# Kernel tuning notes

Hardware: AMD Instinct MI355X
Metric: run time of the kernel (lower is better)

## Reference

```python
import jax, jax.numpy as jnp
import numpy as np

EMBED = 1024
HEADS = 16
HEAD_DIM = EMBED // HEADS


def setup_inputs() -> dict:
    key = jax.random.key(0)
    kx, kq, kk, kv, ko = jax.random.split(key, 5)
    s = 1.0 / np.sqrt(EMBED)
    return {
        "x": jax.random.normal(kx, (4, 2048, EMBED), dtype=jnp.float32),
        "Wq": jax.random.uniform(kq, (EMBED, EMBED), jnp.float32, -s, s),
        "Wk": jax.random.uniform(kk, (EMBED, EMBED), jnp.float32, -s, s),
        "Wv": jax.random.uniform(kv, (EMBED, EMBED), jnp.float32, -s, s),
        "Wo": jax.random.uniform(ko, (EMBED, EMBED), jnp.float32, -s, s),
    }


def reference(x, Wq, Wk, Wv, Wo):
    B, S, E = x.shape
    # nn.Linear computes x @ W.T; weights stored as (out, in)
    q = (x @ Wq.T).reshape(B, S, HEADS, HEAD_DIM).transpose(0, 2, 1, 3)  # [B,H,S,D]
    k = (x @ Wk.T).reshape(B, S, HEADS, HEAD_DIM).transpose(0, 2, 1, 3)
    v = (x @ Wv.T).reshape(B, S, HEADS, HEAD_DIM).transpose(0, 2, 1, 3)
    scores = jnp.einsum("bhsd,bhtd->bhst", q, k) / np.sqrt(HEAD_DIM)  # [B,H,S,S]
    causal = jnp.triu(jnp.ones((S, S), dtype=bool), k=1)
    scores = jnp.where(causal[None, None], -jnp.inf, scores)
    probs = jax.nn.softmax(scores, axis=-1)  # dropout_rate=0 -> identity
    attn = jnp.einsum("bhst,bhtd->bhsd", probs, v)  # [B,H,S,D]
    attn = attn.transpose(0, 2, 1, 3).reshape(B, S, E)
    return attn @ Wo.T
```

## Files before the change

kernel.cpp:

```cpp
#include <hip/hip_runtime.h>

#define EMB 1024
#define NHEADS 16
#define HD 64
#define BATCH 4
#define SEQ 2048
#define MTOK (BATCH*SEQ)

typedef __bf16 bf16x8 __attribute__((ext_vector_type(8)));
typedef __bf16 bf16x4 __attribute__((ext_vector_type(4)));
typedef float  f32x4  __attribute__((ext_vector_type(4)));

#define MFMA16(a,b,c) __builtin_amdgcn_mfma_f32_16x16x32_bf16(a,b,c,0,0,0)

__device__ __forceinline__ void gload_lds16(const __bf16* g, __bf16* l) {
    __builtin_amdgcn_global_load_lds(
        (__attribute__((address_space(1))) void*)(g),
        (__attribute__((address_space(3))) void*)(l), 16, 0, 0);
}

__global__ void cvt_all(const float* __restrict__ x,  const float* __restrict__ wq,
                        const float* __restrict__ wk, const float* __restrict__ wv,
                        const float* __restrict__ wo,
                        __bf16* xb, __bf16* wqb, __bf16* wkb, __bf16* wvb, __bf16* wob) {
    int z = blockIdx.y;
    const float* src = (z == 0) ? x : (z == 1) ? wq : (z == 2) ? wk : (z == 3) ? wv : wo;
    __bf16*      dst = (z == 0) ? xb : (z == 1) ? wqb : (z == 2) ? wkb : (z == 3) ? wvb : wob;
    int n = (z == 0) ? MTOK * EMB : EMB * EMB;
    int i = (blockIdx.x * blockDim.x + threadIdx.x) * 4;
    if (i < n) {
        float4 v = *(const float4*)(src + i);
        bf16x4 o = { (__bf16)v.x, (__bf16)v.y, (__bf16)v.z, (__bf16)v.w };
        *(bf16x4*)(dst + i) = o;
    }
}

__global__ __launch_bounds__(256) void transpose_v(const __bf16* __restrict__ vb,
                                                   __bf16* __restrict__ vt) {
    __shared__ __bf16 t[64 * 72];
    const int tid = threadIdx.x;
    const int bh = blockIdx.y, s0 = blockIdx.x * 64;
    const __bf16* src = vb + ((size_t)bh * SEQ + s0) * HD;
    int sr = tid >> 3, cc = (tid & 7) * 8;
    bf16x8 a0 = *(const bf16x8*)(src + (size_t)sr * HD + cc);
    bf16x8 a1 = *(const bf16x8*)(src + (size_t)(sr + 32) * HD + cc);
    *(bf16x8*)(t + sr * 72 + cc)        = a0;
    *(bf16x8*)(t + (sr + 32) * 72 + cc) = a1;
    __syncthreads();
    int dr = tid >> 3, g = tid & 7;
    __bf16* dstb = vt + (size_t)bh * HD * SEQ + s0;
    #pragma unroll
    for (int it = 0; it < 2; ++it) {
        int d = dr + it * 32;
        bf16x8 o;
        #pragma unroll
        for (int j = 0; j < 8; ++j) o[j] = t[(g * 8 + j) * 72 + d];
        *(bf16x8*)(dstb + (size_t)d * SEQ + g * 8) = o;
    }
}


#define SCHEDB() __builtin_amdgcn_sched_barrier(0)
#define PH_MID()                                                        \
    do { SCHEDB(); __builtin_amdgcn_s_barrier();                        \
         asm volatile("s_waitcnt lgkmcnt(0)" ::: "memory");             \
         SCHEDB(); __builtin_amdgcn_s_setprio(1); } while (0)
#define PH_END()                                                        \
    do { __builtin_amdgcn_s_setprio(0); SCHEDB();                       \
         __builtin_amdgcn_s_barrier(); SCHEDB(); } while (0)
#define PH_END_VM0()                                                    \
    do { __builtin_amdgcn_s_setprio(0); SCHEDB();                       \
         asm volatile("s_waitcnt vmcnt(0)" ::: "memory");               \
         __builtin_amdgcn_s_barrier(); SCHEDB(); } while (0)
#define PH_END_VM2()                                                    \
    do { __builtin_amdgcn_s_setprio(0); SCHEDB();                       \
         asm volatile("s_waitcnt vmcnt(2)" ::: "memory");               \
         __builtin_amdgcn_s_barrier(); SCHEDB(); } while (0)

#define MMAQ(AF, BF, MH, NHI)                                           \
    do {                                                                \
        _Pragma("unroll")                                               \
        for (int m_ = 0; m_ < 4; ++m_) {                                \
            _Pragma("unroll")                                           \
            for (int n_ = 0; n_ < NH; ++n_) {                           \
                f32x4 c_ = acc[(MH)*4 + m_][(NHI)*NH + n_];             \
                c_ = MFMA16(AF[m_][0], BF[n_][0], c_);                  \
                c_ = MFMA16(AF[m_][1], BF[n_][1], c_);                  \
                acc[(MH)*4 + m_][(NHI)*NH + n_] = c_;                   \
            }                                                           \
        }                                                               \
    } while (0)

template<int BN>
__device__ __forceinline__ void gemm8ph(
    const __bf16* __restrict__ Ag,
    const __bf16* __restrict__ Bg,
    __bf16* __restrict__ As, __bf16* __restrict__ Bs,
    f32x4 (&acc)[8][BN/64])
{
    constexpr int NH    = BN / 128;
    constexpr int BSLOT = BN * 64;

    const int tid   = threadIdx.x;
    const int w     = tid >> 6;
    const int mlane = tid & 15;
    const int quad  = (tid >> 4) & 3;
    const int wm    = w >> 2;
    const int wn    = w & 3;

    const int rho = mlane & 7;
    const int e0  = (quad ^ rho) * 8;
    const int aA0 = mlane * 64 + e0;
    const int aB0 = (wn * (BN / 4) + mlane) * 64 + e0;

    const int so = (tid >> 3) * 1024 + (((tid & 7) ^ ((tid >> 3) & 7)) * 8);
    const int sd = (tid & ~63) * 8;

    const auto stA = [&](int slot, int half, int kt) {
        const __bf16* g = Ag + half * 131072 + kt + so;
        __bf16* l = As + slot * 16384 + half * 8192 + sd;
        gload_lds16(g, l);
        gload_lds16(g + 65536, l + 4096);
    };
    const auto stB = [&](int slot, int half, int kt) {
        const __bf16* g = Bg + half * 131072 + kt + so;
        __bf16* l = Bs + slot * BSLOT + half * 8192 + sd;
        gload_lds16(g, l);
        gload_lds16(g + 65536, l + 4096);
    };
    const auto rdA = [&](bf16x8 (&dst)[4][2], int slot, int grp) {
        const __bf16* base = As + slot * 16384 + wm * 8192 + grp * 4096;
        #pragma unroll
        for (int m = 0; m < 4; ++m) {
            dst[m][0] = *(const bf16x8*)(base + m * 1024 + aA0);
            dst[m][1] = *(const bf16x8*)(base + m * 1024 + (aA0 ^ 32));
        }
    };
    const auto rdB = [&](bf16x8 (&dst)[NH][2], int slot, int nh) {
        const __bf16* base = Bs + slot * BSLOT + nh * (NH * 1024);
        #pragma unroll
        for (int n = 0; n < NH; ++n) {
            dst[n][0] = *(const bf16x8*)(base + n * 1024 + aB0);
            dst[n][1] = *(const bf16x8*)(base + n * 1024 + (aB0 ^ 32));
        }
    };

    const f32x4 fz = {0.f, 0.f, 0.f, 0.f};
    #pragma unroll
    for (int i = 0; i < 8; ++i)
        #pragma unroll
        for (int j = 0; j < BN / 64; ++j) acc[i][j] = fz;

    bf16x8 afA[4][2], afB[4][2], bfA[NH][2], bfB[NH][2];

    stA(0, 0, 0); stA(0, 1, 0); stB(0, 0, 0);
    if (BN == 256) stB(0, 1, 0);
    stA(1, 0, 64);
    asm volatile("s_waitcnt vmcnt(2)" ::: "memory");
    SCHEDB(); __builtin_amdgcn_s_barrier(); SCHEDB();

    #pragma unroll 1
    for (int t = 0; t < 8; ++t) {
        const bool last = (t == 7);
        const int ktc1 = t * 128 + 64;
        const int ktn0 = t * 128 + 128;
        const int ktn1 = t * 128 + 192;

        rdA(afA, 0, 0); rdB(bfA, 0, 0);
        stA(1, 1, ktc1);
        PH_MID(); MMAQ(afA, bfA, 0, 0); PH_END();

        rdB(bfB, 0, 1);
        stB(1, 0, ktc1);
        PH_MID(); MMAQ(afA, bfB, 0, 1); PH_END();

        rdA(afB, 0, 1);
        if (BN == 256) stB(1, 1, ktc1);
        PH_MID(); MMAQ(afB, bfB, 1, 1); PH_END();

        if (!last) stA(0, 0, ktn0);
        PH_MID(); MMAQ(afB, bfA, 1, 0);
        if (last) PH_END_VM0(); else PH_END_VM2();

        rdA(afA, 1, 0); rdB(bfA, 1, 0);
        if (!last) stA(0, 1, ktn0);
        PH_MID(); MMAQ(afA, bfA, 0, 0); PH_END();

        rdB(bfB, 1, 1);
        if (!last) stB(0, 0, ktn0);
        PH_MID(); MMAQ(afA, bfB, 0, 1); PH_END();

        rdA(afB, 1, 1);
        if (!last && BN == 256) stB(0, 1, ktn0);
        PH_MID(); MMAQ(afB, bfB, 1, 1); PH_END();

        if (!last) stA(1, 0, ktn1);
        PH_MID(); MMAQ(afB, bfA, 1, 0);
        if (last) PH_END(); else PH_END_VM2();
    }
}

__global__ __launch_bounds__(512, 2) void qkv_gemm(
    const __bf16* __restrict__ xb, const __bf16* __restrict__ wqkv,
    __bf16* __restrict__ Qb, __bf16* __restrict__ Kb, __bf16* __restrict__ Vb)
{
    __shared__ __bf16 As[2 * 256 * 64];
    __shared__ __bf16 Bs[2 * 256 * 64];

    const int bid   = blockIdx.x;
    const int local = bid >> 3;
    const int mt    = (bid & 7) * 4 + (local & 3);
    const int nt    = local >> 2;

    f32x4 acc[8][4];
    gemm8ph<256>(xb + (size_t)mt * 262144, wqkv + (size_t)nt * 262144, As, Bs, acc);

    const int tid = threadIdx.x, w = tid >> 6;
    const int mlane = tid & 15, quad = (tid >> 4) & 3;
    const int wm = w >> 2, wn = w & 3;
    const int rowb = mt * 256 + wm * 128;
    const int colb = nt * 256 + wn * 64;

    #pragma unroll
    for (int ni = 0; ni < 4; ++ni) {
        int gcol = colb + (ni >> 1) * 32 + (ni & 1) * 16 + mlane;
        int z = gcol >> 10, cc = gcol & 1023;
        int h = cc >> 6, d = cc & 63;
        __bf16* O = (z == 0) ? Qb : (z == 1) ? Kb : Vb;
        float scl = (z == 0) ? 0.18033688011112042f : 1.0f;
        #pragma unroll
        for (int mi = 0; mi < 8; ++mi) {
            int grow = rowb + (mi >> 2) * 64 + (mi & 3) * 16 + quad * 4;
            int b = grow >> 11, s = grow & 2047;
            #pragma unroll
            for (int r = 0; r < 4; ++r)
                O[(((size_t)b * NHEADS + h) * SEQ + (s + r)) * HD + d] =
                    (__bf16)(acc[mi][ni][r] * scl);
        }
    }
}

__global__ __launch_bounds__(512, 2) void out_gemm(
    const __bf16* __restrict__ attnb, const __bf16* __restrict__ wo,
    float* __restrict__ out)
{
    __shared__ __bf16 As[2 * 256 * 64];
    __shared__ __bf16 Bs[2 * 128 * 64];

    const int bid   = blockIdx.x;
    const int local = bid >> 3;
    const int mt    = (bid & 7) * 4 + (local & 3);
    const int nt    = local >> 2;

    f32x4 acc[8][2];
    gemm8ph<128>(attnb + (size_t)mt * 262144, wo + (size_t)nt * 131072, As, Bs, acc);

    const int tid = threadIdx.x, w = tid >> 6;
    const int mlane = tid & 15, quad = (tid >> 4) & 3;
    const int wm = w >> 2, wn = w & 3;
    const int rowb = mt * 256 + wm * 128;
    const int colb = nt * 128 + wn * 32;

    #pragma unroll
    for (int mi = 0; mi < 8; ++mi) {
        int grow = rowb + (mi >> 2) * 64 + (mi & 3) * 16 + quad * 4;
        #pragma unroll
        for (int ni = 0; ni < 2; ++ni) {
            int gcol = colb + ni * 16 + mlane;
            #pragma unroll
            for (int r = 0; r < 4; ++r)
                out[(size_t)(grow + r) * EMB + gcol] = acc[mi][ni][r];
        }
    }
}

__global__ __launch_bounds__(512, 1) void attn_kernel(
    const __bf16* __restrict__ Qb, const __bf16* __restrict__ Kb,
    const __bf16* __restrict__ Vtg, __bf16* __restrict__ attnb)
{
    __shared__ __bf16 Ks[2 * 64 * 64];
    __shared__ __bf16 Vs[2 * 64 * 64];
    __shared__ __bf16 Ps[8 * 16 * 72];

    const int tid = threadIdx.x, w = tid >> 6, lane = tid & 63;
    const int mlane = lane & 15, quad = lane >> 4;
    const int h = blockIdx.y, b = blockIdx.z;
    const size_t headoff = ((size_t)b * NHEADS + h) * SEQ * HD;
    const __bf16* Qg = Qb + headoff;
    const __bf16* Kg = Kb + headoff;
    const __bf16* Vg = Vtg + headoff;
    __bf16* Psw = Ps + w * 16 * 72;
    const int g0 = quad ^ (mlane & 7);
    const f32x4 fzero = {0.f, 0.f, 0.f, 0.f};

    const int st_row = tid >> 3;
    const int st_cc  = (tid & 7) ^ (st_row & 7);
    const int st_dst = (tid & ~63) * 8;

    for (int sp = 0; sp < 2; ++sp) {
        const int strip = sp ? (15 - (int)blockIdx.x) : (int)blockIdx.x;
        const int qw  = strip * 128 + w * 16;
        const int nch = 2 * strip + 2;

        __syncthreads();

        gload_lds16(Kg + (size_t)st_row * HD + st_cc * 8, Ks + st_dst);
        gload_lds16(Vg + (size_t)st_row * SEQ + st_cc * 8, Vs + st_dst);

        bf16x8 bq0 = *(const bf16x8*)(Qg + (size_t)(qw + mlane) * HD + quad * 8);
        bf16x8 bq1 = *(const bf16x8*)(Qg + (size_t)(qw + mlane) * HD + 32 + quad * 8);

        float l_acc = 0.f;
        f32x4 o[4];
        #pragma unroll
        for (int dt = 0; dt < 4; ++dt) o[dt] = fzero;

        for (int c = 0; c < nch; ++c) {
            const int tb = c * 64;
            const __bf16* Kp = Ks + (c & 1) * 4096;
            const __bf16* Vp = Vs + (c & 1) * 4096;
            __bf16* Kn = Ks + ((c & 1) ^ 1) * 4096;
            __bf16* Vn = Vs + ((c & 1) ^ 1) * 4096;

            asm volatile("s_waitcnt vmcnt(0)" ::: "memory");
            __syncthreads();

            if (c + 1 < nch) {
                const int tbn = tb + 64;
                gload_lds16(Kg + (size_t)(tbn + st_row) * HD + st_cc * 8, Kn + st_dst);
                gload_lds16(Vg + (size_t)st_row * SEQ + tbn + st_cc * 8, Vn + st_dst);
            }

            const int rel = qw + 15 - tb;
            if (rel >= 0) {
                f32x4 s[4];
                #pragma unroll
                for (int mt = 0; mt < 4; ++mt) {
                    const __bf16* ka = Kp + (mt * 16 + mlane) * 64;
                    bf16x8 ak0 = *(const bf16x8*)(ka + g0 * 8);
                    bf16x8 ak1 = *(const bf16x8*)(ka + (g0 ^ 4) * 8);
                    s[mt] = MFMA16(ak1, bq1, MFMA16(ak0, bq0, fzero));
                }
                if (rel < 78) {
                    const int qrel = qw + mlane - tb - quad * 4;
                    #pragma unroll
                    for (int mt = 0; mt < 4; ++mt)
                        #pragma unroll
                        for (int r = 0; r < 4; ++r)
                            if (mt * 16 + r > qrel) s[mt][r] = -3e38f;
                }

                f32x4 vsum = fzero;
                #pragma unroll
                for (int mt = 0; mt < 4; ++mt) {
                    #pragma unroll
                    for (int r = 0; r < 4; ++r)
                        s[mt][r] = __builtin_amdgcn_exp2f(s[mt][r]);
                    vsum += s[mt];
                    bf16x4 pb = { (__bf16)s[mt][0], (__bf16)s[mt][1],
                                  (__bf16)s[mt][2], (__bf16)s[mt][3] };
                    *(bf16x4*)(Psw + mlane * 72 + mt * 16 + quad * 4) = pb;
                }
                l_acc += (vsum[0] + vsum[1]) + (vsum[2] + vsum[3]);

                #pragma unroll
                for (int ks = 0; ks < 2; ++ks) {
                    bf16x8 ap = *(const bf16x8*)(Psw + mlane * 72 + ks * 32 + quad * 8);
                    #pragma unroll
                    for (int dt = 0; dt < 4; ++dt) {
                        const __bf16* va = Vp + (dt * 16 + mlane) * 64;
                        bf16x8 bv = *(const bf16x8*)(va + (((ks * 4 + quad) ^ (mlane & 7)) * 8));
                        o[dt] = MFMA16(ap, bv, o[dt]);
                    }
                }
            }
        }

        float lf = l_acc;
        lf += __shfl_xor(lf, 16);
        lf += __shfl_xor(lf, 32);
        #pragma unroll
        for (int r = 0; r < 4; ++r) {
            float lr = __shfl(lf, quad * 4 + r);
            float linv = 1.0f / lr;
            int q = qw + quad * 4 + r;
            size_t rowoff = ((size_t)b * SEQ + q) * EMB + h * HD;
            #pragma unroll
            for (int dt = 0; dt < 4; ++dt)
                attnb[rowoff + dt * 16 + mlane] = (__bf16)(o[dt][r] * linv);
        }
    }
}

extern "C" void kernel_launch(void* const* d_in, const int* in_sizes, int n_in,
                              void* d_out, int out_size, void* d_ws, size_t ws_size,
                              hipStream_t stream) {
    const float* x  = (const float*)d_in[0];
    const float* Wq = (const float*)d_in[1];
    const float* Wk = (const float*)d_in[2];
    const float* Wv = (const float*)d_in[3];
    const float* Wo = (const float*)d_in[4];
    float* out = (float*)d_out;

    char* ws = (char*)d_ws;
    __bf16* xb    = (__bf16*)(ws);
    __bf16* wqb   = (__bf16*)(ws + 16777216);
    __bf16* wkb   = (__bf16*)(ws + 18874368);
    __bf16* wvb   = (__bf16*)(ws + 20971520);
    __bf16* wob   = (__bf16*)(ws + 23068672);
    __bf16* qb    = (__bf16*)(ws + 25165824);
    __bf16* kb    = (__bf16*)(ws + 41943040);
    __bf16* vb    = (__bf16*)(ws + 58720256);
    __bf16* attnb = (__bf16*)(ws + 75497472);
    __bf16* vtb   = xb;

    cvt_all<<<dim3(8192, 5), 256, 0, stream>>>(x, Wq, Wk, Wv, Wo, xb, wqb, wkb, wvb, wob);

    qkv_gemm<<<dim3(384), 512, 0, stream>>>(xb, wqb, qb, kb, vb);

    transpose_v<<<dim3(SEQ / 64, BATCH * NHEADS), 256, 0, stream>>>(vb, vtb);

    attn_kernel<<<dim3(8, NHEADS, BATCH), 512, 0, stream>>>(qb, kb, vtb, attnb);

    out_gemm<<<dim3(256), 512, 0, stream>>>(attnb, wob, out);
}
```

Measured before the change: 264.9 us.

## Retile QKV GEMM to 256x192 tiles and compact cvt grid

The QKV projection GEMM moves from 256x256 to 256x192 output tiles with a new six-phase pipelined mainloop, raising the grid from 384 to 512 blocks so it fills the CUs more evenly. The fp32-to-bf16 conversion kernel now uses a flat grid sized exactly to the data instead of a 5-row grid where most weight blocks did nothing. The out-projection GEMM gets its own specialised 128-wide version, and its store loop is reordered. The new QKV tile does less reuse per block, shrinks LDS use and changes the pipeline schedule.

```diff
diff --git a/kernel.cpp b/kernel.cpp
--- a/kernel.cpp
+++ b/kernel.cpp
@@ -23,16 +23,16 @@
                         const float* __restrict__ wk, const float* __restrict__ wv,
                         const float* __restrict__ wo,
                         __bf16* xb, __bf16* wqb, __bf16* wkb, __bf16* wvb, __bf16* wob) {
-    int z = blockIdx.y;
+    int bid = blockIdx.x;
+    int z, rel;
+    if (bid < 8192) { z = 0; rel = bid; }
+    else            { z = 1 + ((bid - 8192) >> 10); rel = (bid - 8192) & 1023; }
     const float* src = (z == 0) ? x : (z == 1) ? wq : (z == 2) ? wk : (z == 3) ? wv : wo;
     __bf16*      dst = (z == 0) ? xb : (z == 1) ? wqb : (z == 2) ? wkb : (z == 3) ? wvb : wob;
-    int n = (z == 0) ? MTOK * EMB : EMB * EMB;
-    int i = (blockIdx.x * blockDim.x + threadIdx.x) * 4;
-    if (i < n) {
-        float4 v = *(const float4*)(src + i);
-        bf16x4 o = { (__bf16)v.x, (__bf16)v.y, (__bf16)v.z, (__bf16)v.w };
-        *(bf16x4*)(dst + i) = o;
-    }
+    int i = (rel * 256 + threadIdx.x) * 4;
+    float4 v = *(const float4*)(src + i);
+    bf16x4 o = { (__bf16)v.x, (__bf16)v.y, (__bf16)v.z, (__bf16)v.w };
+    *(bf16x4*)(dst + i) = o;
 }
 
 __global__ __launch_bounds__(256) void transpose_v(const __bf16* __restrict__ vb,
@@ -59,7 +59,6 @@
     }
 }
 
-
 #define SCHEDB() __builtin_amdgcn_sched_barrier(0)
 #define PH_MID()                                                        \
     do { SCHEDB(); __builtin_amdgcn_s_barrier();                        \
@@ -77,30 +76,31 @@
          asm volatile("s_waitcnt vmcnt(2)" ::: "memory");               \
          __builtin_amdgcn_s_barrier(); SCHEDB(); } while (0)
 
-#define MMAQ(AF, BF, MH, NHI)                                           \
-    do {                                                                \
-        _Pragma("unroll")                                               \
-        for (int m_ = 0; m_ < 4; ++m_) {                                \
-            _Pragma("unroll")                                           \
-            for (int n_ = 0; n_ < NH; ++n_) {                           \
-                f32x4 c_ = acc[(MH)*4 + m_][(NHI)*NH + n_];             \
-                c_ = MFMA16(AF[m_][0], BF[n_][0], c_);                  \
-                c_ = MFMA16(AF[m_][1], BF[n_][1], c_);                  \
-                acc[(MH)*4 + m_][(NHI)*NH + n_] = c_;                   \
-            }                                                           \
-        }                                                               \
-    } while (0)
-
-template<int BN>
-__device__ __forceinline__ void gemm8ph(
+#define MM_N01(AF, G)                                                   \
+    do { _Pragma("unroll") for (int m_ = 0; m_ < 4; ++m_) {             \
+         _Pragma("unroll") for (int n_ = 0; n_ < 2; ++n_) {             \
+            f32x4 c_ = acc[(G)*4 + m_][n_];                             \
+            c_ = MFMA16(AF[m_][0], bfA[n_][0], c_);                     \
+            c_ = MFMA16(AF[m_][1], bfA[n_][1], c_);                     \
+            acc[(G)*4 + m_][n_] = c_; } } } while (0)
+
+#define MM_N2()                                                         \
+    do { _Pragma("unroll") for (int m_ = 0; m_ < 4; ++m_) {             \
+            f32x4 c_ = acc[m_][2];                                      \
+            c_ = MFMA16(afA[m_][0], bfB[0], c_);                        \
+            c_ = MFMA16(afA[m_][1], bfB[1], c_);                        \
+            acc[m_][2] = c_;                                            \
+            f32x4 d_ = acc[4 + m_][2];                                  \
+            d_ = MFMA16(afB[m_][0], bfB[0], d_);                        \
+            d_ = MFMA16(afB[m_][1], bfB[1], d_);                        \
+            acc[4 + m_][2] = d_; } } while (0)
+
+__device__ __forceinline__ void gemm6ph192(
     const __bf16* __restrict__ Ag,
     const __bf16* __restrict__ Bg,
     __bf16* __restrict__ As, __bf16* __restrict__ Bs,
-    f32x4 (&acc)[8][BN/64])
+    f32x4 (&acc)[8][3])
 {
-    constexpr int NH    = BN / 128;
-    constexpr int BSLOT = BN * 64;
-
     const int tid   = threadIdx.x;
     const int w     = tid >> 6;
     const int mlane = tid & 15;
@@ -108,94 +108,86 @@
     const int wm    = w >> 2;
     const int wn    = w & 3;
 
-    const int rho = mlane & 7;
-    const int e0  = (quad ^ rho) * 8;
-    const int aA0 = mlane * 64 + e0;
-    const int aB0 = (wn * (BN / 4) + mlane) * 64 + e0;
+    const int e0  = (quad ^ (mlane & 7)) * 8;
+    const int aB0 = (wn * 48 + mlane) * 64 + e0;
+    const int aB2 = (wn * 48 + 32 + mlane) * 64 + e0;
 
     const int so = (tid >> 3) * 1024 + (((tid & 7) ^ ((tid >> 3) & 7)) * 8);
     const int sd = (tid & ~63) * 8;
 
-    const auto stA = [&](int slot, int half, int kt) {
-        const __bf16* g = Ag + half * 131072 + kt + so;
-        __bf16* l = As + slot * 16384 + half * 8192 + sd;
-        gload_lds16(g, l);
-        gload_lds16(g + 65536, l + 4096);
-    };
-    const auto stB = [&](int slot, int half, int kt) {
-        const __bf16* g = Bg + half * 131072 + kt + so;
-        __bf16* l = Bs + slot * BSLOT + half * 8192 + sd;
-        gload_lds16(g, l);
-        gload_lds16(g + 65536, l + 4096);
-    };
-    const auto rdA = [&](bf16x8 (&dst)[4][2], int slot, int grp) {
+    const auto stA1 = [&](int slot, int c, int kt) {
+        gload_lds16(Ag + c * 65536 + kt + so, As + slot * 16384 + c * 4096 + sd);
+    };
+    const auto stB1 = [&](int slot, int c, int kt) {
+        gload_lds16(Bg + c * 65536 + kt + so, Bs + slot * 12288 + c * 4096 + sd);
+    };
+    const auto rdA2 = [&](bf16x8 (&dst)[4][2], int slot, int grp) {
         const __bf16* base = As + slot * 16384 + wm * 8192 + grp * 4096;
+        const int o0 = mlane * 64 + e0;
         #pragma unroll
         for (int m = 0; m < 4; ++m) {
-            dst[m][0] = *(const bf16x8*)(base + m * 1024 + aA0);
-            dst[m][1] = *(const bf16x8*)(base + m * 1024 + (aA0 ^ 32));
-        }
-    };
-    const auto rdB = [&](bf16x8 (&dst)[NH][2], int slot, int nh) {
-        const __bf16* base = Bs + slot * BSLOT + nh * (NH * 1024);
-        #pragma unroll
-        for (int n = 0; n < NH; ++n) {
+            dst[m][0] = *(const bf16x8*)(base + m * 1024 + o0);
+            dst[m][1] = *(const bf16x8*)(base + m * 1024 + (o0 ^ 32));
+        }
+    };
+    const auto rdB01 = [&](bf16x8 (&dst)[2][2], int slot) {
+        const __bf16* base = Bs + slot * 12288;
+        #pragma unroll
+        for (int n = 0; n < 2; ++n) {
             dst[n][0] = *(const bf16x8*)(base + n * 1024 + aB0);
             dst[n][1] = *(const bf16x8*)(base + n * 1024 + (aB0 ^ 32));
         }
+    };
+    const auto rdB2 = [&](bf16x8 (&dst)[2], int slot) {
+        const __bf16* base = Bs + slot * 12288;
+        dst[0] = *(const bf16x8*)(base + aB2);
+        dst[1] = *(const bf16x8*)(base + (aB2 ^ 32));
     };
 
     const f32x4 fz = {0.f, 0.f, 0.f, 0.f};
     #pragma unroll
     for (int i = 0; i < 8; ++i)
         #pragma unroll
-        for (int j = 0; j < BN / 64; ++j) acc[i][j] = fz;
-
-    bf16x8 afA[4][2], afB[4][2], bfA[NH][2], bfB[NH][2];
-
-    stA(0, 0, 0); stA(0, 1, 0); stB(0, 0, 0);
-    if (BN == 256) stB(0, 1, 0);
-    stA(1, 0, 64);
+        for (int j = 0; j < 3; ++j) acc[i][j] = fz;
+
+    bf16x8 afA[4][2], afB[4][2], bfA[2][2], bfB[2];
+
+    stA1(0, 0, 0); stA1(0, 1, 0); stA1(0, 2, 0); stA1(0, 3, 0);
+    stB1(0, 0, 0); stB1(0, 1, 0); stB1(0, 2, 0);
+    stA1(1, 0, 64); stA1(1, 1, 64);
     asm volatile("s_waitcnt vmcnt(2)" ::: "memory");
     SCHEDB(); __builtin_amdgcn_s_barrier(); SCHEDB();
 
     #pragma unroll 1
     for (int t = 0; t < 8; ++t) {
         const bool last = (t == 7);
-        const int ktc1 = t * 128 + 64;
-        const int ktn0 = t * 128 + 128;
-        const int ktn1 = t * 128 + 192;
-
-        rdA(afA, 0, 0); rdB(bfA, 0, 0);
-        stA(1, 1, ktc1);
-        PH_MID(); MMAQ(afA, bfA, 0, 0); PH_END();
-
-        rdB(bfB, 0, 1);
-        stB(1, 0, ktc1);
-        PH_MID(); MMAQ(afA, bfB, 0, 1); PH_END();
-
-        rdA(afB, 0, 1);
-        if (BN == 256) stB(1, 1, ktc1);
-        PH_MID(); MMAQ(afB, bfB, 1, 1); PH_END();
-
-        if (!last) stA(0, 0, ktn0);
-        PH_MID(); MMAQ(afB, bfA, 1, 0);
+        const int k_s1 = t * 128 + 64;
+        const int k_n0 = t * 128 + 128;
+        const int k_n1 = t * 128 + 192;
+
+        rdA2(afA, 0, 0); rdB01(bfA, 0);
+        stA1(1, 2, k_s1); stA1(1, 3, k_s1);
+        PH_MID(); MM_N01(afA, 0); PH_END();
+
+        rdA2(afB, 0, 1); rdB2(bfB, 0);
+        stB1(1, 0, k_s1); stB1(1, 1, k_s1);
+        PH_MID(); MM_N2(); PH_END();
+
+        stB1(1, 2, k_s1);
+        if (!last) { stA1(0, 0, k_n0); stA1(0, 1, k_n0); }
+        PH_MID(); MM_N01(afB, 1);
         if (last) PH_END_VM0(); else PH_END_VM2();
 
-        rdA(afA, 1, 0); rdB(bfA, 1, 0);
-        if (!last) stA(0, 1, ktn0);
-        PH_MID(); MMAQ(afA, bfA, 0, 0); PH_END();
-
-        rdB(bfB, 1, 1);
-        if (!last) stB(0, 0, ktn0);
-        PH_MID(); MMAQ(afA, bfB, 0, 1); PH_END();
-
-        rdA(afB, 1, 1);
-        if (!last && BN == 256) stB(0, 1, ktn0);
-        PH_MID(); MMAQ(afB, bfB, 1, 1); PH_END();
-
-        if (!last) stA(1, 0, ktn1);
-        PH_MID(); MMAQ(afB, bfA, 1, 0);
+        rdA2(afA, 1, 0); rdB01(bfA, 1);
+        if (!last) { stA1(0, 2, k_n0); stA1(0, 3, k_n0); }
+        PH_MID(); MM_N01(afA, 0); PH_END();
+
+        rdA2(afB, 1, 1); rdB2(bfB, 1);
+        if (!last) { stB1(0, 0, k_n0); stB1(0, 1, k_n0); }
+        PH_MID(); MM_N2(); PH_END();
+
+        if (!last) { stB1(0, 2, k_n0); stA1(1, 0, k_n1); stA1(1, 1, k_n1); }
+        PH_MID(); MM_N01(afB, 1);
         if (last) PH_END(); else PH_END_VM2();
     }
 }
@@ -205,25 +197,25 @@
     __bf16* __restrict__ Qb, __bf16* __restrict__ Kb, __bf16* __restrict__ Vb)
 {
     __shared__ __bf16 As[2 * 256 * 64];
-    __shared__ __bf16 Bs[2 * 256 * 64];
+    __shared__ __bf16 Bs[2 * 192 * 64];
 
     const int bid   = blockIdx.x;
     const int local = bid >> 3;
     const int mt    = (bid & 7) * 4 + (local & 3);
     const int nt    = local >> 2;
 
-    f32x4 acc[8][4];
-    gemm8ph<256>(xb + (size_t)mt * 262144, wqkv + (size_t)nt * 262144, As, Bs, acc);
+    f32x4 acc[8][3];
+    gemm6ph192(xb + (size_t)mt * 262144, wqkv + (size_t)nt * 196608, As, Bs, acc);
 
     const int tid = threadIdx.x, w = tid >> 6;
     const int mlane = tid & 15, quad = (tid >> 4) & 3;
     const int wm = w >> 2, wn = w & 3;
     const int rowb = mt * 256 + wm * 128;
-    const int colb = nt * 256 + wn * 64;
+    const int colb = nt * 192 + wn * 48;
 
     #pragma unroll
-    for (int ni = 0; ni < 4; ++ni) {
-        int gcol = colb + (ni >> 1) * 32 + (ni & 1) * 16 + mlane;
+    for (int ni = 0; ni < 3; ++ni) {
+        int gcol = colb + ni * 16 + mlane;
         int z = gcol >> 10, cc = gcol & 1023;
         int h = cc >> 6, d = cc & 63;
         __bf16* O = (z == 0) ? Qb : (z == 1) ? Kb : Vb;
@@ -240,6 +232,115 @@
     }
 }
 
+#define MMAQ(AF, BF, MH, NHI)                                           \
+    do {                                                                \
+        _Pragma("unroll")                                               \
+        for (int m_ = 0; m_ < 4; ++m_) {                                \
+            f32x4 c_ = acc[(MH)*4 + m_][(NHI)];                         \
+            c_ = MFMA16(AF[m_][0], BF[0][0], c_);                       \
+            c_ = MFMA16(AF[m_][1], BF[0][1], c_);                       \
+            acc[(MH)*4 + m_][(NHI)] = c_;                               \
+        }                                                               \
+    } while (0)
+
+__device__ __forceinline__ void gemm8ph128(
+    const __bf16* __restrict__ Ag,
+    const __bf16* __restrict__ Bg,
+    __bf16* __restrict__ As, __bf16* __restrict__ Bs,
+    f32x4 (&acc)[8][2])
+{
+    const int tid   = threadIdx.x;
+    const int w     = tid >> 6;
+    const int mlane = tid & 15;
+    const int quad  = (tid >> 4) & 3;
+    const int wm    = w >> 2;
+    const int wn    = w & 3;
+
+    const int e0  = (quad ^ (mlane & 7)) * 8;
+    const int aA0 = mlane * 64 + e0;
+    const int aB0 = (wn * 32 + mlane) * 64 + e0;
+
+    const int so = (tid >> 3) * 1024 + (((tid & 7) ^ ((tid >> 3) & 7)) * 8);
+    const int sd = (tid & ~63) * 8;
+
+    const auto stA = [&](int slot, int half, int kt) {
+        const __bf16* g = Ag + half * 131072 + kt + so;
+        __bf16* l = As + slot * 16384 + half * 8192 + sd;
+        gload_lds16(g, l);
+        gload_lds16(g + 65536, l + 4096);
+    };
+    const auto stB = [&](int slot, int kt) {
+        const __bf16* g = Bg + kt + so;
+        __bf16* l = Bs + slot * 8192 + sd;
+        gload_lds16(g, l);
+        gload_lds16(g + 65536, l + 4096);
+    };
+    const auto rdA = [&](bf16x8 (&dst)[4][2], int slot, int grp) {
+        const __bf16* base = As + slot * 16384 + wm * 8192 + grp * 4096;
+        #pragma unroll
+        for (int m = 0; m < 4; ++m) {
+            dst[m][0] = *(const bf16x8*)(base + m * 1024 + aA0);
+            dst[m][1] = *(const bf16x8*)(base + m * 1024 + (aA0 ^ 32));
+        }
+    };
+    const auto rdB = [&](bf16x8 (&dst)[1][2], int slot, int nh) {
+        const __bf16* base = Bs + slot * 8192 + nh * 1024;
+        dst[0][0] = *(const bf16x8*)(base + aB0);
+        dst[0][1] = *(const bf16x8*)(base + (aB0 ^ 32));
+    };
+
+    const f32x4 fz = {0.f, 0.f, 0.f, 0.f};
+    #pragma unroll
+    for (int i = 0; i < 8; ++i)
+        #pragma unroll
+        for (int j = 0; j < 2; ++j) acc[i][j] = fz;
+
+    bf16x8 afA[4][2], afB[4][2], bfA[1][2], bfB[1][2];
+
+    stA(0, 0, 0); stA(0, 1, 0); stB(0, 0);
+    stA(1, 0, 64);
+    asm volatile("s_waitcnt vmcnt(2)" ::: "memory");
+    SCHEDB(); __builtin_amdgcn_s_barrier(); SCHEDB();
+
+    #pragma unroll 1
+    for (int t = 0; t < 8; ++t) {
+        const bool last = (t == 7);
+        const int ktc1 = t * 128 + 64;
+        const int ktn0 = t * 128 + 128;
+        const int ktn1 = t * 128 + 192;
+
+        rdA(afA, 0, 0); rdB(bfA, 0, 0);
+        stA(1, 1, ktc1);
+        PH_MID(); MMAQ(afA, bfA, 0, 0); PH_END();
+
+        rdB(bfB, 0, 1);
+        stB(1, ktc1);
+        PH_MID(); MMAQ(afA, bfB, 0, 1); PH_END();
+
+        rdA(afB, 0, 1);
+        PH_MID(); MMAQ(afB, bfB, 1, 1); PH_END();
+
+        if (!last) stA(0, 0, ktn0);
+        PH_MID(); MMAQ(afB, bfA, 1, 0);
+        if (last) PH_END_VM0(); else PH_END_VM2();
+
+        rdA(afA, 1, 0); rdB(bfA, 1, 0);
+        if (!last) stA(0, 1, ktn0);
+        PH_MID(); MMAQ(afA, bfA, 0, 0); PH_END();
+
+        rdB(bfB, 1, 1);
+        if (!last) stB(0, ktn0);
+        PH_MID(); MMAQ(afA, bfB, 0, 1); PH_END();
+
+        rdA(afB, 1, 1);
+        PH_MID(); MMAQ(afB, bfB, 1, 1); PH_END();
+
+        if (!last) stA(1, 0, ktn1);
+        PH_MID(); MMAQ(afB, bfA, 1, 0);
+        if (last) PH_END(); else PH_END_VM2();
+    }
+}
+
 __global__ __launch_bounds__(512, 2) void out_gemm(
     const __bf16* __restrict__ attnb, const __bf16* __restrict__ wo,
     float* __restrict__ out)
@@ -253,7 +354,7 @@
     const int nt    = local >> 2;
 
     f32x4 acc[8][2];
-    gemm8ph<128>(attnb + (size_t)mt * 262144, wo + (size_t)nt * 131072, As, Bs, acc);
+    gemm8ph128(attnb + (size_t)mt * 262144, wo + (size_t)nt * 131072, As, Bs, acc);
 
     const int tid = threadIdx.x, w = tid >> 6;
     const int mlane = tid & 15, quad = (tid >> 4) & 3;
@@ -265,11 +366,12 @@
     for (int mi = 0; mi < 8; ++mi) {
         int grow = rowb + (mi >> 2) * 64 + (mi & 3) * 16 + quad * 4;
         #pragma unroll
-        for (int ni = 0; ni < 2; ++ni) {
-            int gcol = colb + ni * 16 + mlane;
+        for (int r = 0; r < 4; ++r) {
             #pragma unroll
-            for (int r = 0; r < 4; ++r)
+            for (int ni = 0; ni < 2; ++ni) {
+                int gcol = colb + ni * 16 + mlane;
                 out[(size_t)(grow + r) * EMB + gcol] = acc[mi][ni][r];
+            }
         }
     }
 }
@@ -414,9 +516,9 @@
     __bf16* attnb = (__bf16*)(ws + 75497472);
     __bf16* vtb   = xb;
 
-    cvt_all<<<dim3(8192, 5), 256, 0, stream>>>(x, Wq, Wk, Wv, Wo, xb, wqb, wkb, wvb, wob);
-
-    qkv_gemm<<<dim3(384), 512, 0, stream>>>(xb, wqb, qb, kb, vb);
+    cvt_all<<<dim3(12288), 256, 0, stream>>>(x, Wq, Wk, Wv, Wo, xb, wqb, wkb, wvb, wob);
+
+    qkv_gemm<<<dim3(512), 512, 0, stream>>>(xb, wqb, qb, kb, vb);
 
     transpose_v<<<dim3(SEQ / 64, BATCH * NHEADS), 256, 0, stream>>>(vb, vtb);
 
```

After: 251.1 us. 1.05x faster.
